# Performance work log

Hardware: AMD Instinct MI355X
Metric: run time of the kernel (lower is better)

Reference implementation:

```python
import jax, jax.numpy as jnp
import numpy as np

B, S, D, H, HD = 2, 2048, 768, 12, 64


def setup_inputs() -> dict:
    key = jax.random.key(0)
    ks = jax.random.split(key, 8)
    w = lambda k, shp: jax.random.normal(k, shp, dtype=jnp.float32) * 0.02
    return {
        "hidden_states": jax.random.normal(ks[0], (B, S, D), dtype=jnp.float32),
        "Wq": w(ks[1], (D, D)), "bq": jnp.zeros((D,), jnp.float32),
        "Wk": w(ks[2], (D, D)), "bk": jnp.zeros((D,), jnp.float32),
        "Wv": w(ks[3], (D, D)), "bv": jnp.zeros((D,), jnp.float32),
        # hedgehog feature maps are initialized to identity in the module
        "Wfq": jnp.eye(HD, dtype=jnp.float32) + w(ks[4], (HD, HD)),
        "bfq": jnp.zeros((HD,), jnp.float32),
        "Wfk": jnp.eye(HD, dtype=jnp.float32) + w(ks[5], (HD, HD)),
        "bfk": jnp.zeros((HD,), jnp.float32),
    }


def _heads(x):
    # [B,S,D] -> [B,H,S,HD]
    return x.reshape(B, S, H, HD).transpose(0, 2, 1, 3)


def _feature_map(x, Wf, bf):
    # exp / exp(-x) hedgehog map: [B,H,S,HD] -> [B,H,S,2*HD]
    y = jnp.einsum('bhsd,ed->bhse', x, Wf) + bf
    return jnp.concatenate([jnp.exp(y), jnp.exp(-y)], axis=-1)


def reference(hidden_states, Wq, bq, Wk, bk, Wv, bv, Wfq, bfq, Wfk, bfk):
    h = hidden_states
    q = _heads(h @ Wq.T + bq)   # [B,H,S,HD]
    k = _heads(h @ Wk.T + bk)
    v = _heads(h @ Wv.T + bv)

    # frozen base (softmax) attention producing outputs + true_attns
    scale = 1.0 / np.sqrt(HD).astype(np.float32)
    scores = jnp.einsum('bhmd,bhnd->bhmn', q, k) * scale
    true_attns = jax.nn.softmax(scores, axis=-1)
    out = jnp.einsum('bhmn,bhnd->bhmd', true_attns, v)
    outputs = out.transpose(0, 2, 1, 3).reshape(B, S, D)

    # hedgehog predicted attention: quadratic linear attention
    fq = _feature_map(q, Wfq, bfq)  # [B,H,S,2*HD]
    fk = _feature_map(k, Wfk, bfk)
    qk = jnp.einsum('bhmd,bhnd->bhmn', fq, fk)
    pred_attns = qk / qk.sum(axis=-1, keepdims=True)

    return outputs, pred_attns, true_attns
```

## Files before the change

### kernel.cpp

```cpp
#include <hip/hip_runtime.h>
#include <math.h>

namespace {

constexpr int kB = 2, kS = 2048, kD = 768, kH = 12, kHD = 64, kF = 128, kBH = kB * kH;

typedef __attribute__((ext_vector_type(8))) short short8;
typedef __attribute__((ext_vector_type(4))) short short4v;
typedef __attribute__((ext_vector_type(4))) float f32x4;

__device__ __forceinline__ ushort f2bf(float x) {
    union { float f; unsigned u; } v; v.f = x;
    return (ushort)((v.u + 0x7fffu + ((v.u >> 16) & 1u)) >> 16);
}
__device__ __forceinline__ float bf2f(ushort u) {
    union { unsigned u; float f; } v; v.u = ((unsigned)u) << 16; return v.f;
}

__device__ __forceinline__ void gload16(const ushort* g, void* lds) {
    __builtin_amdgcn_global_load_lds(
        (const __attribute__((address_space(1))) void*)g,
        (__attribute__((address_space(3))) void*)lds, 16, 0, 0);
}

__device__ __forceinline__ void gstage64x64(ushort* ldsBase, const ushort* g,
                                            size_t strideElems, int w, int lane) {
    #pragma unroll
    for (int j = 0; j < 2; ++j) {
        const int row = 16 * w + 8 * j + (lane >> 3);
        const int chunk = lane & 7;
        const ushort* gp = g + (size_t)row * strideElems + ((chunk ^ (row & 7)) * 8);
        void* lp = (char*)ldsBase + (16 * w + 8 * j) * 128;
        gload16(gp, lp);
    }
}

__device__ __forceinline__ void gstage64x128(ushort* ldsBase, const ushort* g,
                                             int w, int lane) {
    #pragma unroll
    for (int j = 0; j < 4; ++j) {
        const int row = 16 * w + 4 * j + (lane >> 4);
        const int chunk = lane & 15;
        const ushort* gp = g + (size_t)row * kF + ((chunk ^ (row & 7)) * 8);
        void* lp = (char*)ldsBase + (16 * w + 4 * j) * 256;
        gload16(gp, lp);
    }
}

__device__ __forceinline__ void stage64x64(ushort* dst, const ushort* srcRow0,
                                           size_t rowStride, int t) {
    const int row = t >> 2, ce = (t & 3) * 16;
    const ushort* s = srcRow0 + (size_t)row * rowStride + ce;
    uint4 u0 = *(const uint4*)s;
    uint4 u1 = *(const uint4*)(s + 8);
    const int sw = (row & 7) << 4;
    *(uint4*)((char*)dst + row * 128 + ((ce * 2) ^ sw)) = u0;
    *(uint4*)((char*)dst + row * 128 + ((ce * 2 + 16) ^ sw)) = u1;
}

__device__ __forceinline__ void stage64x128(ushort* dst, const ushort* srcRow0, int t) {
    const int row = t >> 2, ce = (t & 3) * 32;
    const ushort* s = srcRow0 + (size_t)row * kF + ce;
    const int sw = (row & 7) << 4;
    #pragma unroll
    for (int u = 0; u < 4; ++u) {
        uint4 x = *(const uint4*)(s + u * 8);
        *(uint4*)((char*)dst + row * 256 + ((ce * 2 + u * 16) ^ sw)) = x;
    }
}

__global__ __launch_bounds__(256) void cast_kernel(
    const float* __restrict__ s0, const float* __restrict__ s1,
    const float* __restrict__ s2, const float* __restrict__ s3,
    ushort* __restrict__ d0, ushort* __restrict__ d1,
    ushort* __restrict__ d2, ushort* __restrict__ d3)
{
    const int seg = blockIdx.y;
    const float* src = seg == 0 ? s0 : seg == 1 ? s1 : seg == 2 ? s2 : s3;
    ushort* dst      = seg == 0 ? d0 : seg == 1 ? d1 : seg == 2 ? d2 : d3;
    const int n4 = (seg == 0 ? kB * kS * kD : kD * kD) / 4;
    for (int i = blockIdx.x * 256 + threadIdx.x; i < n4; i += gridDim.x * 256) {
        float4 v = *(const float4*)&src[(size_t)i * 4];
        short4v o;
        o[0] = (short)f2bf(v.x); o[1] = (short)f2bf(v.y);
        o[2] = (short)f2bf(v.z); o[3] = (short)f2bf(v.w);
        *(short4v*)&dst[(size_t)i * 4] = o;
    }
}

__global__ __launch_bounds__(256) void qkv_mfma_kernel(
    const ushort* __restrict__ hb,
    const ushort* __restrict__ Wqb, const ushort* __restrict__ Wkb,
    const ushort* __restrict__ Wvb,
    const float* __restrict__ bq, const float* __restrict__ bk,
    const float* __restrict__ bv,
    ushort* __restrict__ qd, ushort* __restrict__ kd, ushort* __restrict__ vTd)
{
    const int which = blockIdx.z;
    const ushort* __restrict__ Wb  = which == 0 ? Wqb : which == 1 ? Wkb : Wvb;
    const float* __restrict__ bias = which == 0 ? bq : which == 1 ? bk : bv;

    const int m0 = blockIdx.x * 128;
    const int n0 = blockIdx.y * 64;
    const int t = threadIdx.x, lane = t & 63, w = t >> 6;
    const int g = lane >> 4, ln = lane & 15;

    __shared__ __align__(16) ushort As[128 * 64];
    __shared__ __align__(16) ushort Bs[64 * 64];

    f32x4 acc[2][4];
    #pragma unroll
    for (int rs = 0; rs < 2; ++rs)
        #pragma unroll
        for (int nt = 0; nt < 4; ++nt) acc[rs][nt] = (f32x4){0.f, 0.f, 0.f, 0.f};

    for (int k0 = 0; k0 < kD; k0 += 64) {
        __syncthreads();
        #pragma unroll
        for (int u = 0; u < 4; ++u) {
            const int ci = u * 256 + t, row = ci >> 3, c = ci & 7;
            uint4 x = *(const uint4*)&hb[(size_t)(m0 + row) * kD + k0 + c * 8];
            *(uint4*)((char*)As + row * 128 + ((c * 16) ^ ((row & 7) << 4))) = x;
        }
        #pragma unroll
        for (int u = 0; u < 2; ++u) {
            const int ci = u * 256 + t, row = ci >> 3, c = ci & 7;
            uint4 x = *(const uint4*)&Wb[(size_t)(n0 + row) * kD + k0 + c * 8];
            *(uint4*)((char*)Bs + row * 128 + ((c * 16) ^ ((row & 7) << 4))) = x;
        }
        __syncthreads();

        short8 a[2][2], b[4][2];
        #pragma unroll
        for (int rs = 0; rs < 2; ++rs) {
            const int row = 32 * w + 16 * rs + ln, sw = (row & 7) << 4;
            #pragma unroll
            for (int kc = 0; kc < 2; ++kc)
                a[rs][kc] = *(const short8*)((const char*)As + row * 128 + ((kc * 64 + g * 16) ^ sw));
        }
        #pragma unroll
        for (int nt = 0; nt < 4; ++nt) {
            const int rk = nt * 16 + ln, sw = (rk & 7) << 4;
            #pragma unroll
            for (int kc = 0; kc < 2; ++kc)
                b[nt][kc] = *(const short8*)((const char*)Bs + rk * 128 + ((kc * 64 + g * 16) ^ sw));
        }
        #pragma unroll
        for (int rs = 0; rs < 2; ++rs)
            #pragma unroll
            for (int nt = 0; nt < 4; ++nt)
                #pragma unroll
                for (int kc = 0; kc < 2; ++kc)
                    acc[rs][nt] = __builtin_amdgcn_mfma_f32_16x16x32_bf16(
                        a[rs][kc], b[nt][kc], acc[rs][nt], 0, 0, 0);
    }

    const int hh = n0 >> 6;
    float bvn[4];
    #pragma unroll
    for (int nt = 0; nt < 4; ++nt) bvn[nt] = bias[n0 + nt * 16 + ln];

    if (which < 2) {
        ushort* __restrict__ dst = (which == 0) ? qd : kd;
        #pragma unroll
        for (int rs = 0; rs < 2; ++rs)
            #pragma unroll
            for (int nt = 0; nt < 4; ++nt)
                #pragma unroll
                for (int r = 0; r < 4; ++r) {
                    const int m = m0 + 32 * w + 16 * rs + g * 4 + r;
                    const int b_ = m >> 11, s_ = m & (kS - 1);
                    dst[((size_t)(b_ * kH + hh) * kS + s_) * kHD + nt * 16 + ln] =
                        f2bf(acc[rs][nt][r] + bvn[nt]);
                }
    } else {
        #pragma unroll
        for (int rs = 0; rs < 2; ++rs)
            #pragma unroll
            for (int nt = 0; nt < 4; ++nt) {
                const int m = m0 + 32 * w + 16 * rs + g * 4;
                const int b_ = m >> 11, s_ = m & (kS - 1);
                const int d = nt * 16 + ln;
                short4v o;
                #pragma unroll
                for (int r = 0; r < 4; ++r) o[r] = (short)f2bf(acc[rs][nt][r] + bvn[nt]);
                *(short4v*)&vTd[((size_t)(b_ * kH + hh) * kHD + d) * kS + s_] = o;
            }
    }
}

__global__ __launch_bounds__(256) void featmap_kernel(
    const ushort* __restrict__ q, const ushort* __restrict__ k,
    const float* __restrict__ Wfq, const float* __restrict__ bfq,
    const float* __restrict__ Wfk, const float* __restrict__ bfk,
    ushort* __restrict__ fq, ushort* __restrict__ fk)
{
    const int zi = blockIdx.y;
    const ushort* __restrict__ src = zi == 0 ? q : k;
    const float* __restrict__ Wf  = zi == 0 ? Wfq : Wfk;
    const float* __restrict__ bf  = zi == 0 ? bfq : bfk;
    ushort* __restrict__ dst      = zi == 0 ? fq : fk;

    const int row0 = blockIdx.x * 64;
    const int t = threadIdx.x;
    const int lane = t & 63, w = t >> 6;
    const int lrow = t >> 2, lc = (t & 3) * 16;

    __shared__ float Wl[64][65];
    __shared__ float ql[64][68];

    #pragma unroll
    for (int c = 0; c < 16; c += 4) {
        float4 u = *(const float4*)&Wf[(size_t)lrow * 64 + lc + c];
        Wl[lrow][lc + c + 0] = u.x; Wl[lrow][lc + c + 1] = u.y;
        Wl[lrow][lc + c + 2] = u.z; Wl[lrow][lc + c + 3] = u.w;
    }
    {
        union { uint4 v; ushort s[8]; } a0, a1;
        a0.v = *(const uint4*)&src[(size_t)(row0 + lrow) * kHD + lc];
        a1.v = *(const uint4*)&src[(size_t)(row0 + lrow) * kHD + lc + 8];
        float4 f;
        f.x = bf2f(a0.s[0]); f.y = bf2f(a0.s[1]); f.z = bf2f(a0.s[2]); f.w = bf2f(a0.s[3]);
        *(float4*)&ql[lrow][lc] = f;
        f.x = bf2f(a0.s[4]); f.y = bf2f(a0.s[5]); f.z = bf2f(a0.s[6]); f.w = bf2f(a0.s[7]);
        *(float4*)&ql[lrow][lc + 4] = f;
        f.x = bf2f(a1.s[0]); f.y = bf2f(a1.s[1]); f.z = bf2f(a1.s[2]); f.w = bf2f(a1.s[3]);
        *(float4*)&ql[lrow][lc + 8] = f;
        f.x = bf2f(a1.s[4]); f.y = bf2f(a1.s[5]); f.z = bf2f(a1.s[6]); f.w = bf2f(a1.s[7]);
        *(float4*)&ql[lrow][lc + 12] = f;
    }
    __syncthreads();

    float wreg[64];
    #pragma unroll
    for (int d = 0; d < 64; ++d) wreg[d] = Wl[lane][d];
    const float bfv = bf[lane];

    for (int rl = 0; rl < 16; ++rl) {
        const int r = w * 16 + rl;
        float y = bfv;
        #pragma unroll
        for (int d4 = 0; d4 < 64; d4 += 4) {
            float4 qv = *(const float4*)&ql[r][d4];
            y = fmaf(qv.x, wreg[d4 + 0], y);
            y = fmaf(qv.y, wreg[d4 + 1], y);
            y = fmaf(qv.z, wreg[d4 + 2], y);
            y = fmaf(qv.w, wreg[d4 + 3], y);
        }
        const size_t base = (size_t)(row0 + r) * kF;
        dst[base + lane]      = f2bf(__expf(y));
        dst[base + 64 + lane] = f2bf(__expf(-y));
    }
}

__global__ __launch_bounds__(128) void fksum_part_kernel(
    const ushort* __restrict__ fk, float* __restrict__ part)
{
    const int bh = blockIdx.x, g = blockIdx.y, e = threadIdx.x;
    float acc = 0.f;
    const ushort* p = fk + ((size_t)bh * kS + g * 128) * kF + e;
    for (int n = 0; n < 128; ++n) acc += bf2f(p[(size_t)n * kF]);
    part[((size_t)bh * 16 + g) * kF + e] = acc;
}

__global__ __launch_bounds__(128) void fksum_red_kernel(
    const float* __restrict__ part, float* __restrict__ fksum)
{
    const int bh = blockIdx.x, e = threadIdx.x;
    float acc = 0.f;
    for (int g = 0; g < 16; ++g) acc += part[((size_t)bh * 16 + g) * kF + e];
    fksum[bh * kF + e] = acc;
}

__global__ __launch_bounds__(256) void true_attn_kernel(
    const ushort* __restrict__ q, const ushort* __restrict__ k,
    const ushort* __restrict__ vT,
    float* __restrict__ out0, float* __restrict__ out2)
{
    const int orig = blockIdx.y * 32 + blockIdx.x;
    const int swz  = (orig & 7) * 96 + (orig >> 3);
    const int bh = swz >> 5, m0 = (swz & 31) * 64;

    const int t = threadIdx.x, lane = t & 63, w = t >> 6;
    const int g = lane >> 4, ln = lane & 15;

    __shared__ __align__(16) ushort Qs[64 * 64];
    __shared__ __align__(16) ushort Ks[2][64 * 64];
    __shared__ __align__(16) ushort Vs[2][64 * 64];
    __shared__ __align__(16) ushort Ps[64 * 64];

    const ushort* __restrict__ qb = q  + (size_t)bh * kS * kHD;
    const ushort* __restrict__ kb = k  + (size_t)bh * kS * kHD;
    const ushort* __restrict__ vb = vT + (size_t)bh * kHD * kS;

    stage64x64(Qs, qb + (size_t)m0 * kHD, kHD, t);
    __syncthreads();

    short8 aq[2];
    {
        const int row = 16 * w + ln, sw = (row & 7) << 4;
        #pragma unroll
        for (int kc = 0; kc < 2; ++kc)
            aq[kc] = *(const short8*)((const char*)Qs + row * 128 + ((kc * 64 + g * 16) ^ sw));
    }

    gstage64x64(Ks[0], kb, kHD, w, lane);
    float zacc[4] = {0.f, 0.f, 0.f, 0.f};
    for (int tt = 0; tt < 32; ++tt) {
        const int cur = tt & 1;
        if (tt + 1 < 32) {
            gstage64x64(Ks[cur ^ 1], kb + (size_t)(tt + 1) * 64 * kHD, kHD, w, lane);
            asm volatile("s_waitcnt vmcnt(2)" ::: "memory");
        } else {
            asm volatile("s_waitcnt vmcnt(0)" ::: "memory");
        }
        __builtin_amdgcn_sched_barrier(0);
        __builtin_amdgcn_s_barrier();
        const ushort* KsC = Ks[cur];
        #pragma unroll
        for (int nt = 0; nt < 4; ++nt) {
            f32x4 c = {0.f, 0.f, 0.f, 0.f};
            const int rk = nt * 16 + ln, sw = (rk & 7) << 4;
            #pragma unroll
            for (int kc = 0; kc < 2; ++kc) {
                short8 b = *(const short8*)((const char*)KsC + rk * 128 + ((kc * 64 + g * 16) ^ sw));
                c = __builtin_amdgcn_mfma_f32_16x16x32_bf16(aq[kc], b, c, 0, 0, 0);
            }
            #pragma unroll
            for (int r = 0; r < 4; ++r) zacc[r] += __expf(c[r] * 0.125f);
        }
        __builtin_amdgcn_sched_barrier(0);
        __builtin_amdgcn_s_barrier();
    }
    float invl[4];
    #pragma unroll
    for (int r = 0; r < 4; ++r) {
        float z = zacc[r];
        z += __shfl_xor(z, 1); z += __shfl_xor(z, 2);
        z += __shfl_xor(z, 4); z += __shfl_xor(z, 8);
        invl[r] = 1.f / z;
    }

    f32x4 accv[4];
    #pragma unroll
    for (int dt = 0; dt < 4; ++dt) accv[dt] = (f32x4){0.f, 0.f, 0.f, 0.f};

    gstage64x64(Ks[0], kb, kHD, w, lane);
    gstage64x64(Vs[0], vb, kS, w, lane);
    for (int tt = 0; tt < 32; ++tt) {
        const int cur = tt & 1;
        const int n0 = tt * 64;
        if (tt + 1 < 32) {
            gstage64x64(Ks[cur ^ 1], kb + (size_t)(tt + 1) * 64 * kHD, kHD, w, lane);
            gstage64x64(Vs[cur ^ 1], vb + (tt + 1) * 64, kS, w, lane);
            asm volatile("s_waitcnt vmcnt(4)" ::: "memory");
        } else {
            asm volatile("s_waitcnt vmcnt(0)" ::: "memory");
        }
        __builtin_amdgcn_sched_barrier(0);
        __builtin_amdgcn_s_barrier();

        const ushort* KsC = Ks[cur];
        const ushort* VsC = Vs[cur];
        #pragma unroll
        for (int nt = 0; nt < 4; ++nt) {
            f32x4 c = {0.f, 0.f, 0.f, 0.f};
            const int rk = nt * 16 + ln, sw = (rk & 7) << 4;
            #pragma unroll
            for (int kc = 0; kc < 2; ++kc) {
                short8 b = *(const short8*)((const char*)KsC + rk * 128 + ((kc * 64 + g * 16) ^ sw));
                c = __builtin_amdgcn_mfma_f32_16x16x32_bf16(aq[kc], b, c, 0, 0, 0);
            }
            #pragma unroll
            for (int r = 0; r < 4; ++r) {
                const int prow = 16 * w + g * 4 + r;
                const float p = __expf(c[r] * 0.125f) * invl[r];
                out2[((size_t)bh * kS + m0 + prow) * kS + n0 + nt * 16 + ln] = p;
                const int pb = prow * 128 + ((2 * (nt * 16 + ln)) ^ ((prow & 7) << 4));
                *(ushort*)((char*)Ps + pb) = f2bf(p);
            }
        }
        asm volatile("s_waitcnt lgkmcnt(0)" ::: "memory");
        __builtin_amdgcn_sched_barrier(0);
        __builtin_amdgcn_s_barrier();

        const int rowp = 16 * w + ln, swp = (rowp & 7) << 4;
        #pragma unroll
        for (int kc = 0; kc < 2; ++kc) {
            short8 pa = *(const short8*)((const char*)Ps + rowp * 128 + ((kc * 64 + g * 16) ^ swp));
            #pragma unroll
            for (int dt = 0; dt < 4; ++dt) {
                const int rv = dt * 16 + ln, swv = (rv & 7) << 4;
                short8 bv = *(const short8*)((const char*)VsC + rv * 128 + ((kc * 64 + g * 16) ^ swv));
                accv[dt] = __builtin_amdgcn_mfma_f32_16x16x32_bf16(pa, bv, accv[dt], 0, 0, 0);
            }
        }
        __builtin_amdgcn_sched_barrier(0);
        __builtin_amdgcn_s_barrier();
    }

    const int b_ = bh / kH, h_ = bh % kH;
    #pragma unroll
    for (int dt = 0; dt < 4; ++dt)
        #pragma unroll
        for (int r = 0; r < 4; ++r) {
            const int prow = 16 * w + g * 4 + r;
            out0[((size_t)b_ * kS + m0 + prow) * kD + h_ * kHD + dt * 16 + ln] = accv[dt][r];
        }
}

__global__ __launch_bounds__(256) void pred_attn_kernel(
    const ushort* __restrict__ fq, const ushort* __restrict__ fk,
    const float* __restrict__ fksum, float* __restrict__ out1)
{
    const int orig = blockIdx.y * 32 + blockIdx.x;
    const int swz  = (orig & 7) * 96 + (orig >> 3);
    const int bh = swz >> 5, m0 = (swz & 31) * 64;

    const int t = threadIdx.x, lane = t & 63, w = t >> 6;
    const int g = lane >> 4, ln = lane & 15;

    __shared__ __align__(16) ushort Fq[64 * 128];
    __shared__ __align__(16) ushort Fk[2][64 * 128];
    __shared__ float fsum[128];
    __shared__ float invz[64];

    const ushort* __restrict__ fqb = fq + (size_t)bh * kS * kF;
    const ushort* __restrict__ fkb = fk + (size_t)bh * kS * kF;

    stage64x128(Fq, fqb + (size_t)m0 * kF, t);
    if (t < 128) fsum[t] = fksum[bh * kF + t];
    __syncthreads();

    short8 a[4];
    {
        const int row = 16 * w + ln, sw = (row & 7) << 4;
        #pragma unroll
        for (int kc = 0; kc < 4; ++kc)
            a[kc] = *(const short8*)((const char*)Fq + row * 256 + ((kc * 64 + g * 16) ^ sw));
    }

    float den = 0.f;
    #pragma unroll
    for (int kc = 0; kc < 4; ++kc)
        #pragma unroll
        for (int j = 0; j < 8; ++j)
            den += bf2f((ushort)a[kc][j]) * fsum[kc * 32 + g * 8 + j];
    den += __shfl_xor(den, 16);
    den += __shfl_xor(den, 32);
    if (g == 0) invz[16 * w + ln] = 1.f / den;
    __syncthreads();
    float invl[4];
    #pragma unroll
    for (int r = 0; r < 4; ++r) invl[r] = invz[16 * w + g * 4 + r];

    gstage64x128(Fk[0], fkb, w, lane);
    for (int tt = 0; tt < 32; ++tt) {
        const int cur = tt & 1;
        const int n0 = tt * 64;
        if (tt + 1 < 32) {
            gstage64x128(Fk[cur ^ 1], fkb + (size_t)(tt + 1) * 64 * kF, w, lane);
            asm volatile("s_waitcnt vmcnt(4)" ::: "memory");
        } else {
            asm volatile("s_waitcnt vmcnt(0)" ::: "memory");
        }
        __builtin_amdgcn_sched_barrier(0);
        __builtin_amdgcn_s_barrier();

        const ushort* FkC = Fk[cur];
        #pragma unroll
        for (int nt = 0; nt < 4; ++nt) {
            f32x4 c = {0.f, 0.f, 0.f, 0.f};
            const int rk = nt * 16 + ln, sw = (rk & 7) << 4;
            #pragma unroll
            for (int kc = 0; kc < 4; ++kc) {
                short8 b = *(const short8*)((const char*)FkC + rk * 256 + ((kc * 64 + g * 16) ^ sw));
                c = __builtin_amdgcn_mfma_f32_16x16x32_bf16(a[kc], b, c, 0, 0, 0);
            }
            #pragma unroll
            for (int r = 0; r < 4; ++r)
                out1[((size_t)bh * kS + m0 + 16 * w + g * 4 + r) * kS + n0 + nt * 16 + ln] =
                    c[r] * invl[r];
        }
        __builtin_amdgcn_sched_barrier(0);
        __builtin_amdgcn_s_barrier();
    }
}

}

extern "C" void kernel_launch(void* const* d_in, const int* in_sizes, int n_in,
                              void* d_out, int out_size, void* d_ws, size_t ws_size,
                              hipStream_t stream)
{
    (void)in_sizes; (void)n_in; (void)out_size; (void)ws_size;

    const float* hidden = (const float*)d_in[0];
    const float* Wq = (const float*)d_in[1];
    const float* bq = (const float*)d_in[2];
    const float* Wk = (const float*)d_in[3];
    const float* bk = (const float*)d_in[4];
    const float* Wv = (const float*)d_in[5];
    const float* bv = (const float*)d_in[6];
    const float* Wfq = (const float*)d_in[7];
    const float* bfq = (const float*)d_in[8];
    const float* Wfk = (const float*)d_in[9];
    const float* bfk = (const float*)d_in[10];

    float* out = (float*)d_out;
    float* out0 = out;
    float* out1 = out0 + (size_t)kB * kS * kD;
    float* out2 = out1 + (size_t)kBH * kS * kS;

    float* part = (float*)d_ws;
    float* fks  = part + (size_t)kBH * 16 * kF;
    ushort* hb  = (ushort*)(fks + (size_t)kBH * kF);
    ushort* Wqb = hb  + (size_t)kB * kS * kD;
    ushort* Wkb = Wqb + (size_t)kD * kD;
    ushort* Wvb = Wkb + (size_t)kD * kD;
    ushort* qw  = Wvb + (size_t)kD * kD;
    ushort* kw  = qw  + (size_t)kBH * kS * kHD;
    ushort* vTw = kw  + (size_t)kBH * kS * kHD;
    ushort* fqw = vTw + (size_t)kBH * kS * kHD;
    ushort* fkw = fqw + (size_t)kBH * kS * kF;

    cast_kernel<<<dim3(512, 4), 256, 0, stream>>>(
        hidden, Wq, Wk, Wv, hb, Wqb, Wkb, Wvb);
    qkv_mfma_kernel<<<dim3(kB * kS / 128, kD / 64, 3), 256, 0, stream>>>(
        hb, Wqb, Wkb, Wvb, bq, bk, bv, qw, kw, vTw);
    featmap_kernel<<<dim3(kBH * kS / 64, 2), 256, 0, stream>>>(
        qw, kw, Wfq, bfq, Wfk, bfk, fqw, fkw);
    fksum_part_kernel<<<dim3(kBH, 16), 128, 0, stream>>>(fkw, part);
    fksum_red_kernel<<<dim3(kBH), 128, 0, stream>>>(part, fks);
    true_attn_kernel<<<dim3(kS / 64, kBH), 256, 0, stream>>>(qw, kw, vTw, out0, out2);
    pred_attn_kernel<<<dim3(kS / 64, kBH), 256, 0, stream>>>(fqw, fkw, fks, out1);
}
```

Baseline: 318.0 us.

## Swap MFMA operand roles so attention-matrix stores become float4 vectors

Both attention kernels now compute the transposed score tile: K/Fk rows become the A operand and Q/Fq tiles are held in registers as B for all four row groups. Each lane then owns four consecutive columns of one output row, so the huge fp32 attention matrices are written with 16-byte float4 stores instead of scalar stores, and the bf16 P tile is written to LDS as packed 8-byte stores. The cost is more Q-fragment registers per thread, an extra LDS reduction of the softmax row sums across waves, and redundant denominator computation in the predicted-attention kernel.

```diff
diff --git a/kernel.cpp b/kernel.cpp
--- a/kernel.cpp
+++ b/kernel.cpp
@@ -288,6 +288,7 @@
     __shared__ __align__(16) ushort Ks[2][64 * 64];
     __shared__ __align__(16) ushort Vs[2][64 * 64];
     __shared__ __align__(16) ushort Ps[64 * 64];
+    __shared__ float zl[4][64];
 
     const ushort* __restrict__ qb = q  + (size_t)bh * kS * kHD;
     const ushort* __restrict__ kb = k  + (size_t)bh * kS * kHD;
@@ -296,12 +297,13 @@
     stage64x64(Qs, qb + (size_t)m0 * kHD, kHD, t);
     __syncthreads();
 
-    short8 aq[2];
-    {
-        const int row = 16 * w + ln, sw = (row & 7) << 4;
+    short8 bq[4][2];
+    #pragma unroll
+    for (int mt = 0; mt < 4; ++mt) {
+        const int row = mt * 16 + ln, sw = (row & 7) << 4;
         #pragma unroll
         for (int kc = 0; kc < 2; ++kc)
-            aq[kc] = *(const short8*)((const char*)Qs + row * 128 + ((kc * 64 + g * 16) ^ sw));
+            bq[mt][kc] = *(const short8*)((const char*)Qs + row * 128 + ((kc * 64 + g * 16) ^ sw));
     }
 
     gstage64x64(Ks[0], kb, kHD, w, lane);
@@ -317,29 +319,36 @@
         __builtin_amdgcn_sched_barrier(0);
         __builtin_amdgcn_s_barrier();
         const ushort* KsC = Ks[cur];
-        #pragma unroll
-        for (int nt = 0; nt < 4; ++nt) {
+        const int rowa = 16 * w + ln, swa = (rowa & 7) << 4;
+        short8 a0 = *(const short8*)((const char*)KsC + rowa * 128 + ((g * 16) ^ swa));
+        short8 a1 = *(const short8*)((const char*)KsC + rowa * 128 + ((64 + g * 16) ^ swa));
+        #pragma unroll
+        for (int mt = 0; mt < 4; ++mt) {
             f32x4 c = {0.f, 0.f, 0.f, 0.f};
-            const int rk = nt * 16 + ln, sw = (rk & 7) << 4;
-            #pragma unroll
-            for (int kc = 0; kc < 2; ++kc) {
-                short8 b = *(const short8*)((const char*)KsC + rk * 128 + ((kc * 64 + g * 16) ^ sw));
-                c = __builtin_amdgcn_mfma_f32_16x16x32_bf16(aq[kc], b, c, 0, 0, 0);
-            }
-            #pragma unroll
-            for (int r = 0; r < 4; ++r) zacc[r] += __expf(c[r] * 0.125f);
-        }
-        __builtin_amdgcn_sched_barrier(0);
-        __builtin_amdgcn_s_barrier();
-    }
-    float invl[4];
-    #pragma unroll
-    for (int r = 0; r < 4; ++r) {
-        float z = zacc[r];
-        z += __shfl_xor(z, 1); z += __shfl_xor(z, 2);
-        z += __shfl_xor(z, 4); z += __shfl_xor(z, 8);
-        invl[r] = 1.f / z;
-    }
+            c = __builtin_amdgcn_mfma_f32_16x16x32_bf16(a0, bq[mt][0], c, 0, 0, 0);
+            c = __builtin_amdgcn_mfma_f32_16x16x32_bf16(a1, bq[mt][1], c, 0, 0, 0);
+            #pragma unroll
+            for (int r = 0; r < 4; ++r) zacc[mt] += __expf(c[r] * 0.125f);
+        }
+        __builtin_amdgcn_sched_barrier(0);
+        __builtin_amdgcn_s_barrier();
+    }
+    #pragma unroll
+    for (int mt = 0; mt < 4; ++mt) {
+        float z = zacc[mt];
+        z += __shfl_xor(z, 16); z += __shfl_xor(z, 32);
+        zacc[mt] = z;
+    }
+    if (lane < 16) {
+        #pragma unroll
+        for (int mt = 0; mt < 4; ++mt) zl[w][mt * 16 + ln] = zacc[mt];
+    }
+    __syncthreads();
+    float invp[4];
+    #pragma unroll
+    for (int mt = 0; mt < 4; ++mt)
+        invp[mt] = 1.f / (zl[0][mt * 16 + ln] + zl[1][mt * 16 + ln] +
+                          zl[2][mt * 16 + ln] + zl[3][mt * 16 + ln]);
 
     f32x4 accv[4];
     #pragma unroll
@@ -362,23 +371,26 @@
 
         const ushort* KsC = Ks[cur];
         const ushort* VsC = Vs[cur];
-        #pragma unroll
-        for (int nt = 0; nt < 4; ++nt) {
+        const int rowa = 16 * w + ln, swa = (rowa & 7) << 4;
+        short8 a0 = *(const short8*)((const char*)KsC + rowa * 128 + ((g * 16) ^ swa));
+        short8 a1 = *(const short8*)((const char*)KsC + rowa * 128 + ((64 + g * 16) ^ swa));
+        #pragma unroll
+        for (int mt = 0; mt < 4; ++mt) {
             f32x4 c = {0.f, 0.f, 0.f, 0.f};
-            const int rk = nt * 16 + ln, sw = (rk & 7) << 4;
-            #pragma unroll
-            for (int kc = 0; kc < 2; ++kc) {
-                short8 b = *(const short8*)((const char*)KsC + rk * 128 + ((kc * 64 + g * 16) ^ sw));
-                c = __builtin_amdgcn_mfma_f32_16x16x32_bf16(aq[kc], b, c, 0, 0, 0);
-            }
-            #pragma unroll
-            for (int r = 0; r < 4; ++r) {
-                const int prow = 16 * w + g * 4 + r;
-                const float p = __expf(c[r] * 0.125f) * invl[r];
-                out2[((size_t)bh * kS + m0 + prow) * kS + n0 + nt * 16 + ln] = p;
-                const int pb = prow * 128 + ((2 * (nt * 16 + ln)) ^ ((prow & 7) << 4));
-                *(ushort*)((char*)Ps + pb) = f2bf(p);
-            }
+            c = __builtin_amdgcn_mfma_f32_16x16x32_bf16(a0, bq[mt][0], c, 0, 0, 0);
+            c = __builtin_amdgcn_mfma_f32_16x16x32_bf16(a1, bq[mt][1], c, 0, 0, 0);
+            float p0 = __expf(c[0] * 0.125f) * invp[mt];
+            float p1 = __expf(c[1] * 0.125f) * invp[mt];
+            float p2 = __expf(c[2] * 0.125f) * invp[mt];
+            float p3 = __expf(c[3] * 0.125f) * invp[mt];
+            const int mrow = mt * 16 + ln;
+            const size_t ro = ((size_t)bh * kS + m0 + mrow) * kS + n0 + 16 * w + g * 4;
+            *(float4*)&out2[ro] = make_float4(p0, p1, p2, p3);
+            uint2 pk;
+            pk.x = (uint)f2bf(p0) | ((uint)f2bf(p1) << 16);
+            pk.y = (uint)f2bf(p2) | ((uint)f2bf(p3) << 16);
+            const int nb = 32 * w + 8 * g;
+            *(uint2*)((char*)Ps + mrow * 128 + (nb ^ ((mrow & 7) << 4))) = pk;
         }
         asm volatile("s_waitcnt lgkmcnt(0)" ::: "memory");
         __builtin_amdgcn_sched_barrier(0);
@@ -423,7 +435,6 @@
     __shared__ __align__(16) ushort Fq[64 * 128];
     __shared__ __align__(16) ushort Fk[2][64 * 128];
     __shared__ float fsum[128];
-    __shared__ float invz[64];
 
     const ushort* __restrict__ fqb = fq + (size_t)bh * kS * kF;
     const ushort* __restrict__ fkb = fk + (size_t)bh * kS * kF;
@@ -432,27 +443,28 @@
     if (t < 128) fsum[t] = fksum[bh * kF + t];
     __syncthreads();
 
-    short8 a[4];
-    {
-        const int row = 16 * w + ln, sw = (row & 7) << 4;
+    short8 bq[4][4];
+    #pragma unroll
+    for (int mt = 0; mt < 4; ++mt) {
+        const int row = mt * 16 + ln, sw = (row & 7) << 4;
         #pragma unroll
         for (int kc = 0; kc < 4; ++kc)
-            a[kc] = *(const short8*)((const char*)Fq + row * 256 + ((kc * 64 + g * 16) ^ sw));
-    }
-
-    float den = 0.f;
-    #pragma unroll
-    for (int kc = 0; kc < 4; ++kc)
-        #pragma unroll
-        for (int j = 0; j < 8; ++j)
-            den += bf2f((ushort)a[kc][j]) * fsum[kc * 32 + g * 8 + j];
-    den += __shfl_xor(den, 16);
-    den += __shfl_xor(den, 32);
-    if (g == 0) invz[16 * w + ln] = 1.f / den;
-    __syncthreads();
+            bq[mt][kc] = *(const short8*)((const char*)Fq + row * 256 + ((kc * 64 + g * 16) ^ sw));
+    }
+
     float invl[4];
     #pragma unroll
-    for (int r = 0; r < 4; ++r) invl[r] = invz[16 * w + g * 4 + r];
+    for (int mt = 0; mt < 4; ++mt) {
+        float den = 0.f;
+        #pragma unroll
+        for (int kc = 0; kc < 4; ++kc)
+            #pragma unroll
+            for (int j = 0; j < 8; ++j)
+                den += bf2f((ushort)bq[mt][kc][j]) * fsum[kc * 32 + g * 8 + j];
+        den += __shfl_xor(den, 16);
+        den += __shfl_xor(den, 32);
+        invl[mt] = 1.f / den;
+    }
 
     gstage64x128(Fk[0], fkb, w, lane);
     for (int tt = 0; tt < 32; ++tt) {
@@ -468,19 +480,20 @@
         __builtin_amdgcn_s_barrier();
 
         const ushort* FkC = Fk[cur];
-        #pragma unroll
-        for (int nt = 0; nt < 4; ++nt) {
+        const int rowa = 16 * w + ln, swa = (rowa & 7) << 4;
+        short8 a[4];
+        #pragma unroll
+        for (int kc = 0; kc < 4; ++kc)
+            a[kc] = *(const short8*)((const char*)FkC + rowa * 256 + ((kc * 64 + g * 16) ^ swa));
+        #pragma unroll
+        for (int mt = 0; mt < 4; ++mt) {
             f32x4 c = {0.f, 0.f, 0.f, 0.f};
-            const int rk = nt * 16 + ln, sw = (rk & 7) << 4;
-            #pragma unroll
-            for (int kc = 0; kc < 4; ++kc) {
-                short8 b = *(const short8*)((const char*)FkC + rk * 256 + ((kc * 64 + g * 16) ^ sw));
-                c = __builtin_amdgcn_mfma_f32_16x16x32_bf16(a[kc], b, c, 0, 0, 0);
-            }
-            #pragma unroll
-            for (int r = 0; r < 4; ++r)
-                out1[((size_t)bh * kS + m0 + 16 * w + g * 4 + r) * kS + n0 + nt * 16 + ln] =
-                    c[r] * invl[r];
+            #pragma unroll
+            for (int kc = 0; kc < 4; ++kc)
+                c = __builtin_amdgcn_mfma_f32_16x16x32_bf16(a[kc], bq[mt][kc], c, 0, 0, 0);
+            const size_t ro = ((size_t)bh * kS + m0 + mt * 16 + ln) * kS + n0 + 16 * w + g * 4;
+            *(float4*)&out1[ro] = make_float4(c[0] * invl[mt], c[1] * invl[mt],
+                                              c[2] * invl[mt], c[3] * invl[mt]);
         }
         __builtin_amdgcn_sched_barrier(0);
         __builtin_amdgcn_s_barrier();
```

After: 350.3 us. 10.2% more time.

## Fuse hedgehog feature map and fk partial sums into QKV projection epilogue

Applied to the files above, without the earlier changes.

Folds the feature-map projection (now an MFMA over the q/k tile staged in LDS) and the exp(±y) outputs into the QKV GEMM epilogue. The fk column partial sums are reduced in-block, with shuffles and LDS, instead of in a separate kernel. This removes two kernel launches and avoids re-reading q/k and fk from global memory. In exchange the QKV kernel uses more LDS and registers, adds extra syncs, and computes the feature projection in bf16 rather than fp32.

```diff
diff --git a/kernel.cpp b/kernel.cpp
--- a/kernel.cpp
+++ b/kernel.cpp
@@ -94,7 +94,11 @@
     const ushort* __restrict__ Wvb,
     const float* __restrict__ bq, const float* __restrict__ bk,
     const float* __restrict__ bv,
-    ushort* __restrict__ qd, ushort* __restrict__ kd, ushort* __restrict__ vTd)
+    const float* __restrict__ Wfq, const float* __restrict__ bfq,
+    const float* __restrict__ Wfk, const float* __restrict__ bfk,
+    ushort* __restrict__ qd, ushort* __restrict__ kd, ushort* __restrict__ vTd,
+    ushort* __restrict__ fqd, ushort* __restrict__ fkd,
+    float* __restrict__ part)
 {
     const int which = blockIdx.z;
     const ushort* __restrict__ Wb  = which == 0 ? Wqb : which == 1 ? Wkb : Wvb;
@@ -107,6 +111,23 @@
 
     __shared__ __align__(16) ushort As[128 * 64];
     __shared__ __align__(16) ushort Bs[64 * 64];
+    __shared__ __align__(16) ushort Ws[64 * 64];
+    __shared__ float zsum[4][128];
+
+    if (which < 2) {
+        const float* __restrict__ Wf = (which == 0) ? Wfq : Wfk;
+        const int row = t >> 2, ce = (t & 3) * 16;
+        ushort tmp[16];
+        #pragma unroll
+        for (int c = 0; c < 16; c += 4) {
+            float4 u = *(const float4*)&Wf[(size_t)row * 64 + ce + c];
+            tmp[c + 0] = f2bf(u.x); tmp[c + 1] = f2bf(u.y);
+            tmp[c + 2] = f2bf(u.z); tmp[c + 3] = f2bf(u.w);
+        }
+        const int sw = (row & 7) << 4;
+        *(uint4*)((char*)Ws + row * 128 + ((ce * 2) ^ sw)) = *(uint4*)&tmp[0];
+        *(uint4*)((char*)Ws + row * 128 + ((ce * 2 + 16) ^ sw)) = *(uint4*)&tmp[8];
+    }
 
     f32x4 acc[2][4];
     #pragma unroll
@@ -187,80 +208,95 @@
                 *(short4v*)&vTd[((size_t)(b_ * kH + hh) * kHD + d) * kS + s_] = o;
             }
     }
-}
-
-__global__ __launch_bounds__(256) void featmap_kernel(
-    const ushort* __restrict__ q, const ushort* __restrict__ k,
-    const float* __restrict__ Wfq, const float* __restrict__ bfq,
-    const float* __restrict__ Wfk, const float* __restrict__ bfk,
-    ushort* __restrict__ fq, ushort* __restrict__ fk)
-{
-    const int zi = blockIdx.y;
-    const ushort* __restrict__ src = zi == 0 ? q : k;
-    const float* __restrict__ Wf  = zi == 0 ? Wfq : Wfk;
-    const float* __restrict__ bf  = zi == 0 ? bfq : bfk;
-    ushort* __restrict__ dst      = zi == 0 ? fq : fk;
-
-    const int row0 = blockIdx.x * 64;
-    const int t = threadIdx.x;
-    const int lane = t & 63, w = t >> 6;
-    const int lrow = t >> 2, lc = (t & 3) * 16;
-
-    __shared__ float Wl[64][65];
-    __shared__ float ql[64][68];
-
-    #pragma unroll
-    for (int c = 0; c < 16; c += 4) {
-        float4 u = *(const float4*)&Wf[(size_t)lrow * 64 + lc + c];
-        Wl[lrow][lc + c + 0] = u.x; Wl[lrow][lc + c + 1] = u.y;
-        Wl[lrow][lc + c + 2] = u.z; Wl[lrow][lc + c + 3] = u.w;
-    }
-    {
-        union { uint4 v; ushort s[8]; } a0, a1;
-        a0.v = *(const uint4*)&src[(size_t)(row0 + lrow) * kHD + lc];
-        a1.v = *(const uint4*)&src[(size_t)(row0 + lrow) * kHD + lc + 8];
-        float4 f;
-        f.x = bf2f(a0.s[0]); f.y = bf2f(a0.s[1]); f.z = bf2f(a0.s[2]); f.w = bf2f(a0.s[3]);
-        *(float4*)&ql[lrow][lc] = f;
-        f.x = bf2f(a0.s[4]); f.y = bf2f(a0.s[5]); f.z = bf2f(a0.s[6]); f.w = bf2f(a0.s[7]);
-        *(float4*)&ql[lrow][lc + 4] = f;
-        f.x = bf2f(a1.s[0]); f.y = bf2f(a1.s[1]); f.z = bf2f(a1.s[2]); f.w = bf2f(a1.s[3]);
-        *(float4*)&ql[lrow][lc + 8] = f;
-        f.x = bf2f(a1.s[4]); f.y = bf2f(a1.s[5]); f.z = bf2f(a1.s[6]); f.w = bf2f(a1.s[7]);
-        *(float4*)&ql[lrow][lc + 12] = f;
-    }
-    __syncthreads();
-
-    float wreg[64];
-    #pragma unroll
-    for (int d = 0; d < 64; ++d) wreg[d] = Wl[lane][d];
-    const float bfv = bf[lane];
-
-    for (int rl = 0; rl < 16; ++rl) {
-        const int r = w * 16 + rl;
-        float y = bfv;
-        #pragma unroll
-        for (int d4 = 0; d4 < 64; d4 += 4) {
-            float4 qv = *(const float4*)&ql[r][d4];
-            y = fmaf(qv.x, wreg[d4 + 0], y);
-            y = fmaf(qv.y, wreg[d4 + 1], y);
-            y = fmaf(qv.z, wreg[d4 + 2], y);
-            y = fmaf(qv.w, wreg[d4 + 3], y);
-        }
-        const size_t base = (size_t)(row0 + r) * kF;
-        dst[base + lane]      = f2bf(__expf(y));
-        dst[base + 64 + lane] = f2bf(__expf(-y));
-    }
-}
-
-__global__ __launch_bounds__(128) void fksum_part_kernel(
-    const ushort* __restrict__ fk, float* __restrict__ part)
-{
-    const int bh = blockIdx.x, g = blockIdx.y, e = threadIdx.x;
-    float acc = 0.f;
-    const ushort* p = fk + ((size_t)bh * kS + g * 128) * kF + e;
-    for (int n = 0; n < 128; ++n) acc += bf2f(p[(size_t)n * kF]);
-    part[((size_t)bh * 16 + g) * kF + e] = acc;
+
+    if (which < 2) {
+        __syncthreads();
+        #pragma unroll
+        for (int rs = 0; rs < 2; ++rs)
+            #pragma unroll
+            for (int nt = 0; nt < 4; ++nt)
+                #pragma unroll
+                for (int r = 0; r < 4; ++r) {
+                    const int bm = 32 * w + 16 * rs + g * 4 + r;
+                    const int e = nt * 16 + ln;
+                    *(ushort*)((char*)As + bm * 128 + ((2 * e) ^ ((bm & 7) << 4))) =
+                        f2bf(acc[rs][nt][r] + bvn[nt]);
+                }
+        __syncthreads();
+
+        short8 a2[2][2], b2[4][2];
+        #pragma unroll
+        for (int rs = 0; rs < 2; ++rs) {
+            const int row = 32 * w + 16 * rs + ln, sw = (row & 7) << 4;
+            #pragma unroll
+            for (int kc = 0; kc < 2; ++kc)
+                a2[rs][kc] = *(const short8*)((const char*)As + row * 128 + ((kc * 64 + g * 16) ^ sw));
+        }
+        #pragma unroll
+        for (int nt = 0; nt < 4; ++nt) {
+            const int rk = nt * 16 + ln, sw = (rk & 7) << 4;
+            #pragma unroll
+            for (int kc = 0; kc < 2; ++kc)
+                b2[nt][kc] = *(const short8*)((const char*)Ws + rk * 128 + ((kc * 64 + g * 16) ^ sw));
+        }
+        f32x4 yac[2][4];
+        #pragma unroll
+        for (int rs = 0; rs < 2; ++rs)
+            #pragma unroll
+            for (int nt = 0; nt < 4; ++nt) {
+                yac[rs][nt] = (f32x4){0.f, 0.f, 0.f, 0.f};
+                #pragma unroll
+                for (int kc = 0; kc < 2; ++kc)
+                    yac[rs][nt] = __builtin_amdgcn_mfma_f32_16x16x32_bf16(
+                        a2[rs][kc], b2[nt][kc], yac[rs][nt], 0, 0, 0);
+            }
+
+        const float* __restrict__ bf2p = (which == 0) ? bfq : bfk;
+        float bfv[4];
+        #pragma unroll
+        for (int nt = 0; nt < 4; ++nt) bfv[nt] = bf2p[nt * 16 + ln];
+
+        ushort* __restrict__ dstF = (which == 0) ? fqd : fkd;
+        float csp[4] = {0.f, 0.f, 0.f, 0.f}, csm[4] = {0.f, 0.f, 0.f, 0.f};
+        #pragma unroll
+        for (int rs = 0; rs < 2; ++rs)
+            #pragma unroll
+            for (int nt = 0; nt < 4; ++nt)
+                #pragma unroll
+                for (int r = 0; r < 4; ++r) {
+                    const int m = m0 + 32 * w + 16 * rs + g * 4 + r;
+                    const int b_ = m >> 11, s_ = m & (kS - 1);
+                    const float y = yac[rs][nt][r] + bfv[nt];
+                    const ushort hp = f2bf(__expf(y));
+                    const ushort hm = f2bf(__expf(-y));
+                    const size_t base =
+                        ((size_t)(b_ * kH + hh) * kS + s_) * kF + nt * 16 + ln;
+                    dstF[base] = hp;
+                    dstF[base + 64] = hm;
+                    if (which == 1) { csp[nt] += bf2f(hp); csm[nt] += bf2f(hm); }
+                }
+
+        if (which == 1) {
+            #pragma unroll
+            for (int nt = 0; nt < 4; ++nt) {
+                csp[nt] += __shfl_xor(csp[nt], 16); csp[nt] += __shfl_xor(csp[nt], 32);
+                csm[nt] += __shfl_xor(csm[nt], 16); csm[nt] += __shfl_xor(csm[nt], 32);
+            }
+            if (g == 0) {
+                #pragma unroll
+                for (int nt = 0; nt < 4; ++nt) {
+                    zsum[w][nt * 16 + ln]      = csp[nt];
+                    zsum[w][64 + nt * 16 + ln] = csm[nt];
+                }
+            }
+            __syncthreads();
+            if (t < 128) {
+                const float s = zsum[0][t] + zsum[1][t] + zsum[2][t] + zsum[3][t];
+                const int b_ = m0 >> 11, gr = (m0 & (kS - 1)) >> 7;
+                part[((size_t)((b_ * kH + hh) * 16 + gr)) * kF + t] = s;
+            }
+        }
+    }
 }
 
 __global__ __launch_bounds__(128) void fksum_red_kernel(
@@ -527,10 +563,9 @@
     cast_kernel<<<dim3(512, 4), 256, 0, stream>>>(
         hidden, Wq, Wk, Wv, hb, Wqb, Wkb, Wvb);
     qkv_mfma_kernel<<<dim3(kB * kS / 128, kD / 64, 3), 256, 0, stream>>>(
-        hb, Wqb, Wkb, Wvb, bq, bk, bv, qw, kw, vTw);
-    featmap_kernel<<<dim3(kBH * kS / 64, 2), 256, 0, stream>>>(
-        qw, kw, Wfq, bfq, Wfk, bfk, fqw, fkw);
-    fksum_part_kernel<<<dim3(kBH, 16), 128, 0, stream>>>(fkw, part);
+        hb, Wqb, Wkb, Wvb, bq, bk, bv,
+        Wfq, bfq, Wfk, bfk,
+        qw, kw, vTw, fqw, fkw, part);
     fksum_red_kernel<<<dim3(kBH), 128, 0, stream>>>(part, fks);
     true_attn_kernel<<<dim3(kS / 64, kBH), 256, 0, stream>>>(qw, kw, vTw, out0, out2);
     pred_attn_kernel<<<dim3(kS / 64, kBH), 256, 0, stream>>>(fqw, fkw, fks, out1);
```

After: 314.2 us. No clear change (-1.2%).
